# Kernel tuning notes

Measured on AMD Instinct MI355X. Metric: run time of the kernel, lower is better.

## Reference

```python
import jax, jax.numpy as jnp
import numpy as np

# Real Clebsch-Gordan for 1o x 1o -> 2e: orthonormal symmetric-traceless basis
# (matches e3nn component-normalized tensor_product up to basis-sign convention).
_s2 = 1.0 / np.sqrt(2.0)
_s6 = 1.0 / np.sqrt(6.0)
_CG2 = np.zeros((5, 3, 3), np.float32)
_CG2[0, 0, 1] = _CG2[0, 1, 0] = _s2          # xy
_CG2[1, 1, 2] = _CG2[1, 2, 1] = _s2          # yz
_CG2[2, 0, 0] = -_s6; _CG2[2, 1, 1] = -_s6; _CG2[2, 2, 2] = 2 * _s6  # 2z^2-x^2-y^2
_CG2[3, 0, 2] = _CG2[3, 2, 0] = _s2          # xz
_CG2[4, 0, 0] = _s2; _CG2[4, 1, 1] = -_s2    # x^2-y^2
CG2 = jnp.asarray(_CG2)

DEN = 16.0   # denominator init kwarg
EPS = 1e-9


def setup_inputs() -> dict:
    key = jax.random.key(0)
    ks = jax.random.split(key, 16)
    N, E, C = 10000, 160000, 32
    def w(k, fi, fo):
        # e3nn Linear: N(0,1) weights with 1/sqrt(fan_in) path normalization (folded in).
        return jax.random.normal(k, (fi, fo), dtype=jnp.float32) / jnp.sqrt(float(fi))
    return {
        "node_0e": jax.random.normal(ks[0], (N, C), dtype=jnp.float32),
        "node_1o": jax.random.normal(ks[1], (N, C, 3), dtype=jnp.float32),
        "positions": jax.random.normal(ks[2], (N, 3), dtype=jnp.float32),
        "senders": jax.random.randint(ks[3], (E,), 0, N, dtype=jnp.int32),
        "receivers": jax.random.randint(ks[4], (E,), 0, N, dtype=jnp.int32),
        "W_pre_0e": w(ks[5], 2 * C, C),
        "W_pre_1o": w(ks[6], 2 * C, C),
        "W_pre_2e": w(ks[7], C, C),
        "W_post_0e": w(ks[8], C, C),
        "W_post_1o": w(ks[9], C, C),
        "W_post_2e": w(ks[10], C, C),
        "W_sc_0e": w(ks[11], C, C),
        "W_sc_1o": w(ks[12], C, C),
    }


def reference(node_0e, node_1o, positions, senders, receivers,
              W_pre_0e, W_pre_1o, W_pre_2e,
              W_post_0e, W_post_1o, W_post_2e,
              W_sc_0e, W_sc_1o):
    N = positions.shape[0]
    # --- edge update: spherical harmonics (lmax=1, normalize=True, component norm) ---
    rel = positions[receivers] - positions[senders]                       # [E,3]
    sh = jnp.sqrt(3.0) * rel / jnp.maximum(
        jnp.linalg.norm(rel, axis=-1, keepdims=True), EPS)                # 1x1o, [E,3]
    x0 = node_0e[senders]                                                 # [E,C]
    x1 = node_1o[senders]                                                 # [E,C,3]
    # full tensor product sender (x) sh
    tp_1o = x0[:, :, None] * sh[:, None, :]                               # 0e x 1o -> 1o
    tp_0e = jnp.einsum('eci,ei->ec', x1, sh) / jnp.sqrt(3.0)              # 1o x 1o -> 0e
    tp_1e = jnp.cross(x1, sh[:, None, :]) / jnp.sqrt(2.0)                 # 1o x 1o -> 1e
    tp_2e = jnp.einsum('eci,ej,mij->ecm', x1, sh, CG2)                    # 1o x 1o -> 2e
    # message = concatenate([sender, tp]).regroup()
    m0 = jnp.concatenate([x0, tp_0e], axis=1)                             # [E,2C]  0e
    m1 = jnp.concatenate([x1, tp_1o], axis=1)                             # [E,2C,3] 1o
    # --- jraph aggregation: scatter-sum edges into receivers ---
    a0 = jax.ops.segment_sum(m0, receivers, num_segments=N) / DEN         # [N,2C]
    a1 = jax.ops.segment_sum(m1, receivers, num_segments=N) / DEN         # [N,2C,3]
    a2 = jax.ops.segment_sum(tp_2e, receivers, num_segments=N) / DEN      # [N,C,5]
    _ = jax.ops.segment_sum(tp_1e, receivers, num_segments=N)             # 1e dropped by linear_pre (not in target irreps)
    # --- node update ---
    h0 = jax.nn.gelu(a0 @ W_pre_0e)                                       # scalar_activation on 0e only
    h1 = jnp.einsum('nci,cd->ndi', a1, W_pre_1o)
    h2 = jnp.einsum('ncm,cd->ndm', a2, W_pre_2e)
    o0 = h0 @ W_post_0e + node_0e @ W_sc_0e
    o1 = jnp.einsum('nci,cd->ndi', h1, W_post_1o) + jnp.einsum('nci,cd->ndi', node_1o, W_sc_1o)
    o2 = jnp.einsum('ncm,cd->ndm', h2, W_post_2e)  # shortcut 2e block is zero (force_irreps_out)
    return jnp.concatenate([o0, o1.reshape(N, -1), o2.reshape(N, -1)], axis=1)  # [N, 32+96+160]
```

## Files before the change

### kernel.cpp

```cpp
#include <hip/hip_runtime.h>
#include <math.h>

#define C 32
#define OUT_DIM 288
#define MAXDEG 64
#define AGG_ROWS 17
#define AGG_S (AGG_ROWS * 32)

typedef __attribute__((ext_vector_type(8))) short short8v;
typedef __attribute__((ext_vector_type(4))) float float4v;

__device__ __forceinline__ float4v mfma_bf16(short8v a, short8v b, float4v c) {
    return __builtin_amdgcn_mfma_f32_16x16x32_bf16(a, b, c, 0, 0, 0);
}

__device__ __forceinline__ unsigned short f2b(float x) {
    unsigned int u = __float_as_uint(x);
    u = u + 0x7FFFu + ((u >> 16) & 1u);
    return (unsigned short)(u >> 16);
}

__device__ __forceinline__ float gelu_tanh(float x) {
    float x3 = x * x * x;
    float t = tanhf(0.7978845608028654f * (x + 0.044715f * x3));
    return 0.5f * x * (1.0f + t);
}

__global__ void zero_kernel(int* __restrict__ p, int n) {
    int i = blockIdx.x * 256 + threadIdx.x;
    if (i < n) p[i] = 0;
}

__global__ void scatter_sh_kernel(const int* __restrict__ recv,
                                  const int* __restrict__ senders,
                                  const float* __restrict__ pos, int E,
                                  int* __restrict__ counts, float4* __restrict__ adj) {
    int e = blockIdx.x * 256 + threadIdx.x;
    if (e < E) {
        const int r = recv[e];
        const int s = senders[e];
        const float rx = pos[r * 3 + 0] - pos[s * 3 + 0];
        const float ry = pos[r * 3 + 1] - pos[s * 3 + 1];
        const float rz = pos[r * 3 + 2] - pos[s * 3 + 2];
        const float nrm = sqrtf(rx * rx + ry * ry + rz * rz);
        const float f = 1.7320508075688772f / fmaxf(nrm, 1e-9f);
        const int p = atomicAdd(&counts[r], 1);
        if (p < MAXDEG)
            adj[(size_t)r * MAXDEG + p] = make_float4(rx * f, ry * f, rz * f, __int_as_float(s));
    }
}

__global__ __launch_bounds__(256) void edge_agg_kernel(
    const float* __restrict__ node0, const float* __restrict__ node1,
    const int* __restrict__ counts, const float4* __restrict__ adj,
    unsigned short* __restrict__ aggb, int N)
{
    const int tid  = threadIdx.x;
    const int wv   = tid >> 6;
    const int lane = tid & 63;
    const int half = lane >> 5;
    const int c    = lane & 31;
    const int node = blockIdx.x * 4 + wv;
    const bool valid = (node < N);

    const float S2 = 0.70710678118654752f;
    const float S6 = 0.40824829046386302f;
    const float INV_SQRT3 = 0.57735026918962576f;
    const float INV_DEN = 1.0f / 16.0f;

    float ax0 = 0.f, atp0 = 0.f;
    float ax1x = 0.f, ax1y = 0.f, ax1z = 0.f;
    float at1x = 0.f, at1y = 0.f, at1z = 0.f;
    float a2v0 = 0.f, a2v1 = 0.f, a2v2 = 0.f, a2v3 = 0.f, a2v4 = 0.f;

#define EDGE_ACC(A, X0, U1)                                                 \
    {                                                                       \
        const float shx = (A).x, shy = (A).y, shz = (A).z;                  \
        ax0 += (X0);                                                        \
        atp0 += (U1).x * shx + (U1).y * shy + (U1).z * shz;                 \
        ax1x += (U1).x; ax1y += (U1).y; ax1z += (U1).z;                     \
        at1x += (X0) * shx; at1y += (X0) * shy; at1z += (X0) * shz;         \
        a2v0 += S2 * ((U1).x * shy + (U1).y * shx);                         \
        a2v1 += S2 * ((U1).y * shz + (U1).z * shy);                         \
        a2v2 += S6 * (2.f * (U1).z * shz - (U1).x * shx - (U1).y * shy);    \
        a2v3 += S2 * ((U1).x * shz + (U1).z * shx);                         \
        a2v4 += S2 * ((U1).x * shx - (U1).y * shy);                         \
    }

    if (valid) {
        const int deg = min(counts[node], MAXDEG);
        const int beg = node * MAXDEG;
        const int end = beg + deg;
        int k = beg + half;
        while (k + 2 < end) {
            const float4 A0 = adj[k];
            const float4 A1 = adj[k + 2];
            const int b0 = __float_as_int(A0.w) * C + c;
            const int b1 = __float_as_int(A1.w) * C + c;
            const float q0 = node0[b0];
            const float q1 = node0[b1];
            const float3 u0 = *(const float3*)(node1 + b0 * 3);
            const float3 u1 = *(const float3*)(node1 + b1 * 3);
            EDGE_ACC(A0, q0, u0);
            EDGE_ACC(A1, q1, u1);
            k += 4;
        }
        if (k < end) {
            const float4 A0 = adj[k];
            const int b0 = __float_as_int(A0.w) * C + c;
            const float q0 = node0[b0];
            const float3 u0 = *(const float3*)(node1 + b0 * 3);
            EDGE_ACC(A0, q0, u0);
        }
    }
#undef EDGE_ACC

    ax0  += __shfl_xor(ax0, 32, 64);
    atp0 += __shfl_xor(atp0, 32, 64);
    ax1x += __shfl_xor(ax1x, 32, 64);
    ax1y += __shfl_xor(ax1y, 32, 64);
    ax1z += __shfl_xor(ax1z, 32, 64);
    at1x += __shfl_xor(at1x, 32, 64);
    at1y += __shfl_xor(at1y, 32, 64);
    at1z += __shfl_xor(at1z, 32, 64);
    a2v0 += __shfl_xor(a2v0, 32, 64);
    a2v1 += __shfl_xor(a2v1, 32, 64);
    a2v2 += __shfl_xor(a2v2, 32, 64);
    a2v3 += __shfl_xor(a2v3, 32, 64);
    a2v4 += __shfl_xor(a2v4, 32, 64);

    if (valid) {
        float x0n = node0[node * C + c];
        const float3 xu = *(const float3*)(node1 + (node * C + c) * 3);

        unsigned short* ag = aggb + (size_t)node * AGG_S + c;
        if (half == 0) {
            ag[0 * 32]  = f2b(ax0 * INV_DEN);
            ag[1 * 32]  = f2b(atp0 * (INV_DEN * INV_SQRT3));
            ag[2 * 32]  = f2b(ax1x * INV_DEN);
            ag[3 * 32]  = f2b(ax1y * INV_DEN);
            ag[4 * 32]  = f2b(ax1z * INV_DEN);
            ag[5 * 32]  = f2b(at1x * INV_DEN);
            ag[6 * 32]  = f2b(at1y * INV_DEN);
            ag[13 * 32] = f2b(x0n);
            ag[14 * 32] = f2b(xu.x);
        } else {
            ag[7 * 32]  = f2b(at1z * INV_DEN);
            ag[8 * 32]  = f2b(a2v0 * INV_DEN);
            ag[9 * 32]  = f2b(a2v1 * INV_DEN);
            ag[10 * 32] = f2b(a2v2 * INV_DEN);
            ag[11 * 32] = f2b(a2v3 * INV_DEN);
            ag[12 * 32] = f2b(a2v4 * INV_DEN);
            ag[15 * 32] = f2b(xu.y);
            ag[16 * 32] = f2b(xu.z);
        }
    }
}

__global__ __launch_bounds__(256) void node_mfma_kernel(
    const unsigned short* __restrict__ aggb,
    const float* __restrict__ Wpre0, const float* __restrict__ Wpre1,
    const float* __restrict__ Wpre2,
    const float* __restrict__ Wpost0, const float* __restrict__ Wpost1,
    const float* __restrict__ Wpost2,
    const float* __restrict__ Wsc0, const float* __restrict__ Wsc1,
    float* __restrict__ out, int N, int ntiles)
{
    __shared__ unsigned short tr[4][16][48];

    const int wv   = threadIdx.x >> 6;
    const int wave = blockIdx.x * 4 + wv;
    const int tile = __builtin_amdgcn_readfirstlane(wave / 9);
    const int t    = __builtin_amdgcn_readfirstlane(wave % 9);
    if (tile >= ntiles) return;

    const int lane = threadIdx.x & 63;
    const int r    = lane & 15;
    const int kg   = lane >> 4;
    const int k0   = kg * 8;

    const float *Wp1, *Wp2 = nullptr, *Wq1, *Wq2 = nullptr;
    int rowA1, rowA2 = -1, rowX = -1, obase, ostride;
    if (t == 0) {
        rowA1 = 0; rowA2 = 1; rowX = 13;
        Wp1 = Wpre0; Wp2 = Wpre0 + 1024; Wq1 = Wpost0; Wq2 = Wsc0;
        obase = 0; ostride = 1;
    } else if (t <= 3) {
        const int i = t - 1;
        rowA1 = 2 + i; rowA2 = 5 + i; rowX = 14 + i;
        Wp1 = Wpre1; Wp2 = Wpre1 + 1024; Wq1 = Wpost1; Wq2 = Wsc1;
        obase = 32 + i; ostride = 3;
    } else {
        const int m = t - 4;
        rowA1 = 8 + m;
        Wp1 = Wpre2; Wq1 = Wpost2;
        obase = 128 + m; ostride = 5;
    }

    short8v bp1[2], bp2[2], bq1[2], bq2[2];
#pragma unroll
    for (int dt = 0; dt < 2; ++dt) {
        const int d = dt * 16 + r;
#pragma unroll
        for (int j = 0; j < 8; ++j) {
            bp1[dt][j] = (short)f2b(Wp1[(k0 + j) * 32 + d]);
            bq1[dt][j] = (short)f2b(Wq1[(k0 + j) * 32 + d]);
        }
    }
    if (rowA2 >= 0) {
#pragma unroll
        for (int dt = 0; dt < 2; ++dt) {
            const int d = dt * 16 + r;
#pragma unroll
            for (int j = 0; j < 8; ++j) {
                bp2[dt][j] = (short)f2b(Wp2[(k0 + j) * 32 + d]);
                bq2[dt][j] = (short)f2b(Wq2[(k0 + j) * 32 + d]);
            }
        }
    }

    const int node = tile * 16 + r;
    const int nclamp = node < N ? node : (N - 1);
    const unsigned short* ap = aggb + (size_t)nclamp * AGG_S;

    float4v acc0 = {0.f, 0.f, 0.f, 0.f};
    float4v acc1 = {0.f, 0.f, 0.f, 0.f};
    {
        const short8v a1 = *(const short8v*)(ap + rowA1 * 32 + k0);
        acc0 = mfma_bf16(a1, bp1[0], acc0);
        acc1 = mfma_bf16(a1, bp1[1], acc1);
    }
    if (rowA2 >= 0) {
        const short8v a2 = *(const short8v*)(ap + rowA2 * 32 + k0);
        acc0 = mfma_bf16(a2, bp2[0], acc0);
        acc1 = mfma_bf16(a2, bp2[1], acc1);
    }
    if (t == 0) {
#pragma unroll
        for (int q = 0; q < 4; ++q) {
            acc0[q] = gelu_tanh(acc0[q]);
            acc1[q] = gelu_tanh(acc1[q]);
        }
    }

#pragma unroll
    for (int q = 0; q < 4; ++q) {
        tr[wv][kg * 4 + q][r]      = f2b(acc0[q]);
        tr[wv][kg * 4 + q][16 + r] = f2b(acc1[q]);
    }
    asm volatile("s_waitcnt lgkmcnt(0)" ::: "memory");
    __builtin_amdgcn_sched_barrier(0);

    const short8v ha = *(const short8v*)&tr[wv][r][k0];
    float4v o0 = {0.f, 0.f, 0.f, 0.f};
    float4v o1 = {0.f, 0.f, 0.f, 0.f};
    o0 = mfma_bf16(ha, bq1[0], o0);
    o1 = mfma_bf16(ha, bq1[1], o1);
    if (rowX >= 0) {
        const short8v xa = *(const short8v*)(ap + rowX * 32 + k0);
        o0 = mfma_bf16(xa, bq2[0], o0);
        o1 = mfma_bf16(xa, bq2[1], o1);
    }

#pragma unroll
    for (int q = 0; q < 4; ++q) {
        const int nodeo = tile * 16 + kg * 4 + q;
        if (nodeo < N) {
            float* po = out + (size_t)nodeo * OUT_DIM + obase;
            po[r * ostride]        = o0[q];
            po[(16 + r) * ostride] = o1[q];
        }
    }
}

extern "C" void kernel_launch(void* const* d_in, const int* in_sizes, int n_in,
                              void* d_out, int out_size, void* d_ws, size_t ws_size,
                              hipStream_t stream) {
    const float* node0   = (const float*)d_in[0];
    const float* node1   = (const float*)d_in[1];
    const float* pos     = (const float*)d_in[2];
    const int*   senders = (const int*)d_in[3];
    const int*   recv    = (const int*)d_in[4];
    const float* Wpre0   = (const float*)d_in[5];
    const float* Wpre1   = (const float*)d_in[6];
    const float* Wpre2   = (const float*)d_in[7];
    const float* Wpost0  = (const float*)d_in[8];
    const float* Wpost1  = (const float*)d_in[9];
    const float* Wpost2  = (const float*)d_in[10];
    const float* Wsc0    = (const float*)d_in[11];
    const float* Wsc1    = (const float*)d_in[12];
    float* out = (float*)d_out;

    const int N = in_sizes[2] / 3;
    const int E = in_sizes[3];

    int* counts = (int*)d_ws;
    size_t adj_off = ((size_t)N * sizeof(int) + 15) & ~(size_t)15;
    float4* adj = (float4*)((char*)d_ws + adj_off);
    unsigned short* aggb = (unsigned short*)((char*)d_ws + adj_off + (size_t)N * MAXDEG * sizeof(float4));

    zero_kernel<<<(N + 255) / 256, 256, 0, stream>>>(counts, N);
    scatter_sh_kernel<<<(E + 255) / 256, 256, 0, stream>>>(recv, senders, pos, E, counts, adj);
    edge_agg_kernel<<<(N + 3) / 4, 256, 0, stream>>>(node0, node1, counts, adj, aggb, N);

    const int ntiles = (N + 15) / 16;
    const int nwaves = ntiles * 9;
    node_mfma_kernel<<<(nwaves + 3) / 4, 256, 0, stream>>>(
        aggb,
        Wpre0, Wpre1, Wpre2, Wpost0, Wpost1, Wpost2, Wsc0, Wsc1,
        out, N, ntiles);
}
```

Before: 51.92 us.

## Split edge aggregation across two waves per node and pre-convert weights to bf16

The edge aggregation kernel now gives each node two waves, each walking half of the adjacency list with stride 8. Partial sums are combined through shared memory after a block barrier. The CG scale constants are moved out of the per-edge loop into the final writeout. A new small kernel converts and transposes all weight matrices to bf16 once, so each MFMA wave loads its B fragments as packed short8 vectors instead of converting 32 scattered floats per fragment. This adds an extra launch and shared-memory traffic in exchange for more memory-level parallelism on the gather.

Result: no change. 52.43 us (+1.0%).

```diff
diff --git a/kernel.cpp b/kernel.cpp
--- a/kernel.cpp
+++ b/kernel.cpp
@@ -29,6 +29,36 @@
 __global__ void zero_kernel(int* __restrict__ p, int n) {
     int i = blockIdx.x * 256 + threadIdx.x;
     if (i < n) p[i] = 0;
+}
+
+__global__ void wprep_kernel(const float* __restrict__ Wpre0,
+                             const float* __restrict__ Wpre1,
+                             const float* __restrict__ Wpre2,
+                             const float* __restrict__ Wpost0,
+                             const float* __restrict__ Wpost1,
+                             const float* __restrict__ Wpost2,
+                             const float* __restrict__ Wsc0,
+                             const float* __restrict__ Wsc1,
+                             unsigned short* __restrict__ wt) {
+    const int b = blockIdx.x;
+    const float* src;
+    switch (b) {
+        case 0: src = Wpre0;        break;
+        case 1: src = Wpre0 + 1024; break;
+        case 2: src = Wpre1;        break;
+        case 3: src = Wpre1 + 1024; break;
+        case 4: src = Wpre2;        break;
+        case 5: src = Wpost0;       break;
+        case 6: src = Wpost1;       break;
+        case 7: src = Wpost2;       break;
+        case 8: src = Wsc0;         break;
+        default: src = Wsc1;        break;
+    }
+    unsigned short* dst = wt + b * 1024;
+    for (int i = threadIdx.x; i < 1024; i += 256) {
+        const int cc = i >> 5, dd = i & 31;
+        dst[dd * 32 + cc] = f2b(src[cc * 32 + dd]);
+    }
 }
 
 __global__ void scatter_sh_kernel(const int* __restrict__ recv,
@@ -55,13 +85,17 @@
     const int* __restrict__ counts, const float4* __restrict__ adj,
     unsigned short* __restrict__ aggb, int N)
 {
-    const int tid  = threadIdx.x;
-    const int wv   = tid >> 6;
-    const int lane = tid & 63;
-    const int half = lane >> 5;
-    const int c    = lane & 31;
-    const int node = blockIdx.x * 4 + wv;
-    const bool valid = (node < N);
+    __shared__ float prt[2][2][13][32];
+
+    const int tid     = threadIdx.x;
+    const int wv      = tid >> 6;
+    const int slot    = wv >> 1;
+    const int portion = wv & 1;
+    const int lane    = tid & 63;
+    const int half    = lane >> 5;
+    const int c       = lane & 31;
+    const int node    = blockIdx.x * 2 + slot;
+    const bool valid  = (node < N);
 
     const float S2 = 0.70710678118654752f;
     const float S6 = 0.40824829046386302f;
@@ -80,21 +114,21 @@
         atp0 += (U1).x * shx + (U1).y * shy + (U1).z * shz;                 \
         ax1x += (U1).x; ax1y += (U1).y; ax1z += (U1).z;                     \
         at1x += (X0) * shx; at1y += (X0) * shy; at1z += (X0) * shz;         \
-        a2v0 += S2 * ((U1).x * shy + (U1).y * shx);                         \
-        a2v1 += S2 * ((U1).y * shz + (U1).z * shy);                         \
-        a2v2 += S6 * (2.f * (U1).z * shz - (U1).x * shx - (U1).y * shy);    \
-        a2v3 += S2 * ((U1).x * shz + (U1).z * shx);                         \
-        a2v4 += S2 * ((U1).x * shx - (U1).y * shy);                         \
+        a2v0 += (U1).x * shy + (U1).y * shx;                                \
+        a2v1 += (U1).y * shz + (U1).z * shy;                                \
+        a2v2 += 2.f * (U1).z * shz - (U1).x * shx - (U1).y * shy;           \
+        a2v3 += (U1).x * shz + (U1).z * shx;                                \
+        a2v4 += (U1).x * shx - (U1).y * shy;                                \
     }
 
     if (valid) {
         const int deg = min(counts[node], MAXDEG);
         const int beg = node * MAXDEG;
         const int end = beg + deg;
-        int k = beg + half;
-        while (k + 2 < end) {
+        int k = beg + portion * 2 + half;
+        while (k + 4 < end) {
             const float4 A0 = adj[k];
-            const float4 A1 = adj[k + 2];
+            const float4 A1 = adj[k + 4];
             const int b0 = __float_as_int(A0.w) * C + c;
             const int b1 = __float_as_int(A1.w) * C + c;
             const float q0 = node0[b0];
@@ -103,7 +137,7 @@
             const float3 u1 = *(const float3*)(node1 + b1 * 3);
             EDGE_ACC(A0, q0, u0);
             EDGE_ACC(A1, q1, u1);
-            k += 4;
+            k += 8;
         }
         if (k < end) {
             const float4 A0 = adj[k];
@@ -129,41 +163,68 @@
     a2v3 += __shfl_xor(a2v3, 32, 64);
     a2v4 += __shfl_xor(a2v4, 32, 64);
 
+    if (half == 0) {
+        float* p = &prt[slot][portion][0][c];
+        p[0 * 32]  = ax0;
+        p[1 * 32]  = atp0;
+        p[2 * 32]  = ax1x;
+        p[3 * 32]  = ax1y;
+        p[4 * 32]  = ax1z;
+        p[5 * 32]  = at1x;
+        p[6 * 32]  = at1y;
+        p[7 * 32]  = at1z;
+        p[8 * 32]  = a2v0;
+        p[9 * 32]  = a2v1;
+        p[10 * 32] = a2v2;
+        p[11 * 32] = a2v3;
+        p[12 * 32] = a2v4;
+    }
+    __syncthreads();
+
     if (valid) {
-        float x0n = node0[node * C + c];
-        const float3 xu = *(const float3*)(node1 + (node * C + c) * 3);
-
         unsigned short* ag = aggb + (size_t)node * AGG_S + c;
-        if (half == 0) {
-            ag[0 * 32]  = f2b(ax0 * INV_DEN);
-            ag[1 * 32]  = f2b(atp0 * (INV_DEN * INV_SQRT3));
-            ag[2 * 32]  = f2b(ax1x * INV_DEN);
-            ag[3 * 32]  = f2b(ax1y * INV_DEN);
-            ag[4 * 32]  = f2b(ax1z * INV_DEN);
-            ag[5 * 32]  = f2b(at1x * INV_DEN);
-            ag[6 * 32]  = f2b(at1y * INV_DEN);
-            ag[13 * 32] = f2b(x0n);
-            ag[14 * 32] = f2b(xu.x);
+        const float SA = INV_DEN;
+        const float SB = INV_DEN * INV_SQRT3;
+        const float S2D = S2 * INV_DEN;
+        const float S6D = S6 * INV_DEN;
+#define PRT(j) (prt[slot][0][j][c] + prt[slot][1][j][c])
+        if (portion == 0) {
+            if (half == 0) {
+                ag[0 * 32] = f2b(PRT(0) * SA);
+                ag[1 * 32] = f2b(PRT(1) * SB);
+                ag[2 * 32] = f2b(PRT(2) * SA);
+                ag[3 * 32] = f2b(PRT(3) * SA);
+                ag[4 * 32] = f2b(PRT(4) * SA);
+                ag[5 * 32] = f2b(PRT(5) * SA);
+                ag[6 * 32] = f2b(PRT(6) * SA);
+            } else {
+                ag[7 * 32]  = f2b(PRT(7) * SA);
+                ag[8 * 32]  = f2b(PRT(8) * S2D);
+                ag[9 * 32]  = f2b(PRT(9) * S2D);
+                ag[10 * 32] = f2b(PRT(10) * S6D);
+                ag[11 * 32] = f2b(PRT(11) * S2D);
+                ag[12 * 32] = f2b(PRT(12) * S2D);
+            }
         } else {
-            ag[7 * 32]  = f2b(at1z * INV_DEN);
-            ag[8 * 32]  = f2b(a2v0 * INV_DEN);
-            ag[9 * 32]  = f2b(a2v1 * INV_DEN);
-            ag[10 * 32] = f2b(a2v2 * INV_DEN);
-            ag[11 * 32] = f2b(a2v3 * INV_DEN);
-            ag[12 * 32] = f2b(a2v4 * INV_DEN);
-            ag[15 * 32] = f2b(xu.y);
-            ag[16 * 32] = f2b(xu.z);
-        }
+            if (half == 0) {
+                const float x0n = node0[node * C + c];
+                const float x1x = node1[(node * C + c) * 3 + 0];
+                ag[13 * 32] = f2b(x0n);
+                ag[14 * 32] = f2b(x1x);
+            } else {
+                const float x1y = node1[(node * C + c) * 3 + 1];
+                const float x1z = node1[(node * C + c) * 3 + 2];
+                ag[15 * 32] = f2b(x1y);
+                ag[16 * 32] = f2b(x1z);
+            }
+        }
+#undef PRT
     }
 }
 
 __global__ __launch_bounds__(256) void node_mfma_kernel(
     const unsigned short* __restrict__ aggb,
-    const float* __restrict__ Wpre0, const float* __restrict__ Wpre1,
-    const float* __restrict__ Wpre2,
-    const float* __restrict__ Wpost0, const float* __restrict__ Wpost1,
-    const float* __restrict__ Wpost2,
-    const float* __restrict__ Wsc0, const float* __restrict__ Wsc1,
+    const unsigned short* __restrict__ wt,
     float* __restrict__ out, int N, int ntiles)
 {
     __shared__ unsigned short tr[4][16][48];
@@ -179,21 +240,23 @@
     const int kg   = lane >> 4;
     const int k0   = kg * 8;
 
-    const float *Wp1, *Wp2 = nullptr, *Wq1, *Wq2 = nullptr;
+    const unsigned short *pb1, *pb2 = nullptr, *qb1, *qb2 = nullptr;
     int rowA1, rowA2 = -1, rowX = -1, obase, ostride;
     if (t == 0) {
         rowA1 = 0; rowA2 = 1; rowX = 13;
-        Wp1 = Wpre0; Wp2 = Wpre0 + 1024; Wq1 = Wpost0; Wq2 = Wsc0;
+        pb1 = wt + 0 * 1024; pb2 = wt + 1 * 1024;
+        qb1 = wt + 5 * 1024; qb2 = wt + 8 * 1024;
         obase = 0; ostride = 1;
     } else if (t <= 3) {
         const int i = t - 1;
         rowA1 = 2 + i; rowA2 = 5 + i; rowX = 14 + i;
-        Wp1 = Wpre1; Wp2 = Wpre1 + 1024; Wq1 = Wpost1; Wq2 = Wsc1;
+        pb1 = wt + 2 * 1024; pb2 = wt + 3 * 1024;
+        qb1 = wt + 6 * 1024; qb2 = wt + 9 * 1024;
         obase = 32 + i; ostride = 3;
     } else {
         const int m = t - 4;
         rowA1 = 8 + m;
-        Wp1 = Wpre2; Wq1 = Wpost2;
+        pb1 = wt + 4 * 1024; qb1 = wt + 7 * 1024;
         obase = 128 + m; ostride = 5;
     }
 
@@ -201,21 +264,15 @@
 #pragma unroll
     for (int dt = 0; dt < 2; ++dt) {
         const int d = dt * 16 + r;
-#pragma unroll
-        for (int j = 0; j < 8; ++j) {
-            bp1[dt][j] = (short)f2b(Wp1[(k0 + j) * 32 + d]);
-            bq1[dt][j] = (short)f2b(Wq1[(k0 + j) * 32 + d]);
-        }
+        bp1[dt] = *(const short8v*)(pb1 + d * 32 + k0);
+        bq1[dt] = *(const short8v*)(qb1 + d * 32 + k0);
     }
     if (rowA2 >= 0) {
 #pragma unroll
         for (int dt = 0; dt < 2; ++dt) {
             const int d = dt * 16 + r;
-#pragma unroll
-            for (int j = 0; j < 8; ++j) {
-                bp2[dt][j] = (short)f2b(Wp2[(k0 + j) * 32 + d]);
-                bq2[dt][j] = (short)f2b(Wq2[(k0 + j) * 32 + d]);
-            }
+            bp2[dt] = *(const short8v*)(pb2 + d * 32 + k0);
+            bq2[dt] = *(const short8v*)(qb2 + d * 32 + k0);
         }
     }
 
@@ -298,15 +355,16 @@
     size_t adj_off = ((size_t)N * sizeof(int) + 15) & ~(size_t)15;
     float4* adj = (float4*)((char*)d_ws + adj_off);
     unsigned short* aggb = (unsigned short*)((char*)d_ws + adj_off + (size_t)N * MAXDEG * sizeof(float4));
-
+    unsigned short* wt = aggb + (size_t)N * AGG_S;
+
+    wprep_kernel<<<10, 256, 0, stream>>>(
+        Wpre0, Wpre1, Wpre2, Wpost0, Wpost1, Wpost2, Wsc0, Wsc1, wt);
     zero_kernel<<<(N + 255) / 256, 256, 0, stream>>>(counts, N);
     scatter_sh_kernel<<<(E + 255) / 256, 256, 0, stream>>>(recv, senders, pos, E, counts, adj);
-    edge_agg_kernel<<<(N + 3) / 4, 256, 0, stream>>>(node0, node1, counts, adj, aggb, N);
+    edge_agg_kernel<<<(N + 1) / 2, 256, 0, stream>>>(node0, node1, counts, adj, aggb, N);
 
     const int ntiles = (N + 15) / 16;
     const int nwaves = ntiles * 9;
     node_mfma_kernel<<<(nwaves + 3) / 4, 256, 0, stream>>>(
-        aggb,
-        Wpre0, Wpre1, Wpre2, Wpost0, Wpost1, Wpost2, Wsc0, Wsc1,
-        out, N, ntiles);
-}
+        aggb, wt, out, N, ntiles);
+}
```
